# Performance work log

Measured on AMD Instinct MI355X. Metric: run time of the kernel, lower is better.

Reference implementation:

```python
import jax, jax.numpy as jnp
import numpy as np

N_U = 50000
N_I = 50000
E = 800000
HID = 64
HEADS = 4
OUT = 32
NEG_SLOPE = 0.2


def _gat(xs, xd, e, ws, wd, a_s, a_d, b, heads, ch, n_dst, concat):
    # xs:[Ns,Fin] xd:[Nd,Fin] e:[2,E]; PyG GATConv (no self loops, eval mode)
    hs = (xs @ ws).reshape(-1, heads, ch)  # [Ns,H,C]
    hd = (xd @ wd).reshape(-1, heads, ch)  # [Nd,H,C]
    al_s = jnp.einsum('nhc,hc->nh', hs, a_s)  # [Ns,H]
    al_d = jnp.einsum('nhc,hc->nh', hd, a_d)  # [Nd,H]
    src, dst = e[0], e[1]
    alpha = jax.nn.leaky_relu(al_s[src] + al_d[dst], NEG_SLOPE)  # [E,H]
    m = jax.lax.stop_gradient(jax.ops.segment_max(alpha, dst, num_segments=n_dst))
    ealpha = jnp.exp(alpha - m[dst])
    denom = jax.ops.segment_sum(ealpha, dst, num_segments=n_dst)
    coef = ealpha / (denom[dst] + 1e-16)  # segment softmax over incoming edges
    msg = hs[src] * coef[:, :, None]  # [E,H,C]
    out = jax.ops.segment_sum(msg, dst, num_segments=n_dst)  # [Nd,H,C]
    out = out.reshape(n_dst, heads * ch) if concat else out.mean(axis=1)
    return out + b


def _forward(x_user, x_item, e_u2i, e_i2u,
             p_user_w, p_user_b, p_item_w, p_item_b,
             l0_u2i_ws, l0_u2i_wd, l0_u2i_as, l0_u2i_ad, l0_u2i_b,
             l0_i2u_ws, l0_i2u_wd, l0_i2u_as, l0_i2u_ad, l0_i2u_b,
             l1_u2i_ws, l1_u2i_wd, l1_u2i_as, l1_u2i_ad, l1_u2i_b,
             l1_i2u_ws, l1_i2u_wd, l1_i2u_as, l1_i2u_ad, l1_i2u_b):
    hu = jax.nn.elu(x_user @ p_user_w + p_user_b)
    hi = jax.nn.elu(x_item @ p_item_w + p_item_b)
    # layer 0: heads=4, concat=True, out dim HID*HEADS; HeteroConv sum (one edge type per dst)
    hi1 = _gat(hu, hi, e_u2i, l0_u2i_ws, l0_u2i_wd, l0_u2i_as, l0_u2i_ad, l0_u2i_b, HEADS, HID, N_I, True)
    hu1 = _gat(hi, hu, e_i2u, l0_i2u_ws, l0_i2u_wd, l0_i2u_as, l0_i2u_ad, l0_i2u_b, HEADS, HID, N_U, True)
    hu1 = jax.nn.elu(hu1)  # dropout is identity in eval mode
    hi1 = jax.nn.elu(hi1)
    # layer 1: heads=1, concat=False -> mean over heads
    hi2 = _gat(hu1, hi1, e_u2i, l1_u2i_ws, l1_u2i_wd, l1_u2i_as, l1_u2i_ad, l1_u2i_b, 1, OUT, N_I, False)
    hu2 = _gat(hi1, hu1, e_i2u, l1_i2u_ws, l1_i2u_wd, l1_i2u_as, l1_i2u_ad, l1_i2u_b, 1, OUT, N_U, False)
    return hu2, hi2


def setup_inputs() -> dict:
    key = jax.random.key(0)
    ks = jax.random.split(key, 32)
    s = 0.1
    d = {
        'x_user': jax.random.normal(ks[0], (N_U, 128), jnp.float32),
        'x_item': jax.random.normal(ks[1], (N_I, 128), jnp.float32),
        'e_u2i': jax.random.randint(ks[2], (2, E), 0, 50000, jnp.int32),
        'e_i2u': jax.random.randint(ks[3], (2, E), 0, 50000, jnp.int32),
        'p_user_w': jax.random.normal(ks[4], (128, HID), jnp.float32) * s,
        'p_user_b': jax.random.normal(ks[5], (HID,), jnp.float32) * s,
        'p_item_w': jax.random.normal(ks[6], (128, HID), jnp.float32) * s,
        'p_item_b': jax.random.normal(ks[7], (HID,), jnp.float32) * s,
    }
    i = 8
    for lname, fin, h, c in (('l0', HID, HEADS, HID), ('l1', HID * HEADS, 1, OUT)):
        for et in ('u2i', 'i2u'):
            odim = h * c if lname == 'l0' else c
            d[f'{lname}_{et}_ws'] = jax.random.normal(ks[i], (fin, h * c), jnp.float32) * s; i += 1
            d[f'{lname}_{et}_wd'] = jax.random.normal(ks[i], (fin, h * c), jnp.float32) * s; i += 1
            d[f'{lname}_{et}_as'] = jax.random.normal(ks[i], (h, c), jnp.float32) * s; i += 1
            d[f'{lname}_{et}_ad'] = jax.random.normal(ks[i], (h, c), jnp.float32) * s; i += 1
            d[f'{lname}_{et}_b'] = jax.random.normal(ks[i], (odim,), jnp.float32) * s; i += 1
    return d


def reference(x_user, x_item, e_u2i, e_i2u,
              p_user_w, p_user_b, p_item_w, p_item_b,
              l0_u2i_ws, l0_u2i_wd, l0_u2i_as, l0_u2i_ad, l0_u2i_b,
              l0_i2u_ws, l0_i2u_wd, l0_i2u_as, l0_i2u_ad, l0_i2u_b,
              l1_u2i_ws, l1_u2i_wd, l1_u2i_as, l1_u2i_ad, l1_u2i_b,
              l1_i2u_ws, l1_i2u_wd, l1_i2u_as, l1_i2u_ad, l1_i2u_b):
    return _forward(x_user, x_item, e_u2i, e_i2u,
                    p_user_w, p_user_b, p_item_w, p_item_b,
                    l0_u2i_ws, l0_u2i_wd, l0_u2i_as, l0_u2i_ad, l0_u2i_b,
                    l0_i2u_ws, l0_i2u_wd, l0_i2u_as, l0_i2u_ad, l0_i2u_b,
                    l1_u2i_ws, l1_u2i_wd, l1_u2i_as, l1_u2i_ad, l1_u2i_b,
                    l1_i2u_ws, l1_i2u_wd, l1_i2u_as, l1_i2u_ad, l1_i2u_b)
```

## Files before the change

### kernel.cpp

```cpp
#include <hip/hip_runtime.h>
#include <cstdint>
#include <cstddef>

#define NN 50000
#define NE 800000
#define GB 196
#define TILE1 4096
#define CAP 8192

typedef __attribute__((ext_vector_type(8))) short short8;
typedef __attribute__((ext_vector_type(4))) float floatx4;

__device__ __forceinline__ float lrelu_f(float x){ return x >= 0.f ? x : 0.2f*x; }
__device__ __forceinline__ float elu_f(float x){ return x > 0.f ? x : __expf(x) - 1.f; }

__device__ __forceinline__ unsigned short f2bf(float f){
  unsigned int u = __float_as_uint(f);
  u += 0x7FFFu + ((u >> 16) & 1u);
  return (unsigned short)(u >> 16);
}
__device__ __forceinline__ float bf2f(unsigned int us){
  return __uint_as_float(us << 16);
}
__device__ __forceinline__ float4 bf4_load(const unsigned short* p){
  uint2 q = *(const uint2*)p;
  return make_float4(bf2f(q.x & 0xffffu), bf2f(q.x >> 16),
                     bf2f(q.y & 0xffffu), bf2f(q.y >> 16));
}
__device__ __forceinline__ uint2 bf4_pack(float4 o){
  uint2 p;
  p.x = (unsigned)f2bf(o.x) | ((unsigned)f2bf(o.y) << 16);
  p.y = (unsigned)f2bf(o.z) | ((unsigned)f2bf(o.w) << 16);
  return p;
}
__device__ __forceinline__ void split_bf(float a, unsigned short& h, unsigned short& l){
  h = f2bf(a);
  l = f2bf(a - bf2f(h));
}

__device__ __forceinline__ float dot2bf(float acc, unsigned a, unsigned b){
  asm("v_dot2_f32_bf16 %0, %1, %2, %0" : "+v"(acc) : "v"(a), "v"(b));
  return acc;
}

__global__ __launch_bounds__(256) void ghist_kernel(const int* __restrict__ e0,
                                                    const int* __restrict__ e1,
                                                    int* __restrict__ ghist){
  const int ty = blockIdx.y;
  const int* e = ty ? e1 : e0;
  __shared__ int h[GB];
  for (int j=threadIdx.x; j<GB; j+=256) h[j]=0;
  __syncthreads();
  for (int i = blockIdx.x*256 + threadIdx.x; i < NE; i += 256*256)
    atomicAdd(&h[e[NE+i]>>8], 1);
  __syncthreads();
  for (int j=threadIdx.x; j<GB; j+=256) if (h[j]) atomicAdd(&ghist[ty*200+j], h[j]);
}

__global__ __launch_bounds__(256) void gscan_kernel(const int* __restrict__ ghist,
                                                    int* __restrict__ gbase,
                                                    int* __restrict__ gcur){
  __shared__ int wb[4];
  const int t = threadIdx.x, wv = t>>6, l = t&63;
  for (int ty=0; ty<2; ++ty){
    int v = (t < GB) ? ghist[ty*200+t] : 0;
    int sum = v;
    #pragma unroll
    for (int off=1; off<64; off<<=1){
      int x = __shfl_up(sum, off, 64);
      if (l >= off) sum += x;
    }
    if (l == 63) wb[wv] = sum;
    __syncthreads();
    int wbase = 0;
    #pragma unroll
    for (int w=0; w<4; ++w) if (w < wv) wbase += wb[w];
    int excl = wbase + sum - v;
    if (t <= GB) gbase[ty*200+t] = excl;
    if (t <  GB) gcur [ty*200+t] = excl;
    __syncthreads();
  }
}

__global__ __launch_bounds__(256) void part1_kernel(const int* __restrict__ e0,
                                                    const int* __restrict__ e1,
                                                    int* __restrict__ gcur,
                                                    int2* __restrict__ p0,
                                                    int2* __restrict__ p1){
  const int ty = blockIdx.y;
  const int* e = ty ? e1 : e0;
  int2* pairs = ty ? p1 : p0;
  __shared__ int cnt[256];
  __shared__ int lstart[256];
  __shared__ int lcur[256];
  __shared__ int curg[GB];
  __shared__ int lsrc[TILE1];
  __shared__ int ldst[TILE1];
  __shared__ int wb[4];
  const int t = threadIdx.x;
  cnt[t] = 0;
  __syncthreads();
  int dreg[16], sreg[16];
  const int base = blockIdx.x*TILE1;
  const int ntile = min(TILE1, NE - base);
  #pragma unroll
  for (int it=0; it<16; ++it){
    int i = base + it*256 + t;
    int d = -1, s = 0;
    if (i < NE){ d = e[NE+i]; s = e[i]; atomicAdd(&cnt[d>>8], 1); }
    dreg[it] = d; sreg[it] = s;
  }
  __syncthreads();
  int c = cnt[t], sum = c;
  #pragma unroll
  for (int off=1; off<64; off<<=1){
    int x = __shfl_up(sum, off, 64);
    if ((t&63) >= off) sum += x;
  }
  if ((t&63) == 63) wb[t>>6] = sum;
  __syncthreads();
  int wbase = 0;
  #pragma unroll
  for (int w=0; w<4; ++w) if (w < (t>>6)) wbase += wb[w];
  int excl = wbase + sum - c;
  lstart[t] = excl;
  lcur[t] = excl;
  if (t < GB && c > 0) curg[t] = atomicAdd(&gcur[ty*200+t], c);
  __syncthreads();
  #pragma unroll
  for (int it=0; it<16; ++it){
    int d = dreg[it];
    if (d >= 0){
      int pos = atomicAdd(&lcur[d>>8], 1);
      lsrc[pos] = sreg[it];
      ldst[pos] = d;
    }
  }
  __syncthreads();
  for (int i=t; i<ntile; i+=256){
    int d = ldst[i];
    int j = d>>8;
    pairs[curg[j] + (i - lstart[j])] = make_int2(lsrc[i], d);
  }
}

struct Part2Job {
  const int2* pairs; const int* gbase;
  const float* als; const float* ald;
  int* ssrc; int* offs; unsigned short* coef;
};
__global__ __launch_bounds__(256) void part2_kernel(Part2Job j0, Part2Job j1){
  const Part2Job jb = blockIdx.y ? j1 : j0;
  const int b = blockIdx.x;
  const int t = threadIdx.x;
  __shared__ int lcnt[256];
  __shared__ int lcur[256];
  __shared__ int wb[4];
  __shared__ int sorted_src[CAP];
  __shared__ unsigned char sorted_dl[CAP];
  const int gb0 = jb.gbase[b], gb1 = jb.gbase[b+1];
  const int n = gb1 - gb0;
  lcnt[t] = 0;
  __syncthreads();
  for (int i=t; i<n; i+=256)
    atomicAdd(&lcnt[jb.pairs[gb0+i].y - (b<<8)], 1);
  __syncthreads();
  int c = lcnt[t], sum = c;
  #pragma unroll
  for (int off=1; off<64; off<<=1){
    int x = __shfl_up(sum, off, 64);
    if ((t&63) >= off) sum += x;
  }
  if ((t&63) == 63) wb[t>>6] = sum;
  __syncthreads();
  int wbase = 0;
  #pragma unroll
  for (int w=0; w<4; ++w) if (w < (t>>6)) wbase += wb[w];
  int excl = wbase + sum - c;
  lcur[t] = excl;
  int g = (b<<8) + t;
  if (g <= NN) jb.offs[g] = gb0 + excl;
  __syncthreads();
  for (int i=t; i<n; i+=256){
    int2 pr = jb.pairs[gb0+i];
    int dl = pr.y - (b<<8);
    int pos = atomicAdd(&lcur[dl], 1);
    sorted_src[pos] = pr.x;
    sorted_dl[pos] = (unsigned char)dl;
  }
  __syncthreads();
  const float4* als4 = (const float4*)jb.als;
  const float4* ald4 = (const float4*)jb.ald;
  for (int i=t; i<n; i+=256){
    int s  = sorted_src[i];
    int dl = sorted_dl[i];
    float4 a  = als4[s];
    float4 ad = ald4[(b<<8)+dl];
    float4 w;
    w.x = __expf(lrelu_f(a.x+ad.x));
    w.y = __expf(lrelu_f(a.y+ad.y));
    w.z = __expf(lrelu_f(a.z+ad.z));
    w.w = __expf(lrelu_f(a.w+ad.w));
    ((uint2*)jb.coef)[gb0+i] = bf4_pack(w);
    jb.ssrc[gb0+i] = s;
  }
}

struct MgJob {
  const void* A; const float* W; const float* bias;
  void* C; float* outA; float* outB;
  const float* cwS; const float* cwD;
};
template<int NT, bool ELU, bool BF16OUT, bool BF16A, bool LG, bool LOGIT>
__global__ __launch_bounds__(256) void mgemm_kernel(MgJob j0, MgJob j1,
                                                    int M, int K, int N)
{
  const MgJob jb = blockIdx.z ? j1 : j0;
  constexpr int TN = NT*16;
  __shared__ __align__(16) unsigned short Ah[64*72];
  __shared__ __align__(16) unsigned short Al[BF16A ? 8 : 64*72];
  __shared__ __align__(16) unsigned short Bh[TN*72];
  __shared__ __align__(16) unsigned short Bl[TN*72];
  __shared__ float CwS[LOGIT ? 256 : 1];
  __shared__ float CwD[LOGIT ? 256 : 1];
  const int t = threadIdx.x;
  const int m0 = blockIdx.x*64;
  const int n0 = blockIdx.y*TN;
  const int wv = t>>6, l = t&63;
  const int lr = l&15, lq = l>>4;
  if constexpr (LOGIT){ CwS[t] = jb.cwS[t]; CwD[t] = jb.cwD[t]; }
  floatx4 acc[NT];
  #pragma unroll
  for (int i=0;i<NT;i++) acc[i] = (floatx4){0.f,0.f,0.f,0.f};

  for (int kt=0; kt<K; kt+=64){
    if constexpr (BF16A){
      const unsigned short* A = (const unsigned short*)jb.A;
      #pragma unroll
      for (int i=0;i<2;i++){
        int li = t + i*256;
        int r = li >> 3, c8 = (li & 7)*8;
        short8 v = {0,0,0,0,0,0,0,0};
        if (m0 + r < M) v = *(const short8*)(A + (size_t)(m0+r)*K + kt + c8);
        *(short8*)&Ah[r*72 + c8] = v;
      }
    } else {
      const float* A = (const float*)jb.A;
      #pragma unroll
      for (int i=0;i<4;i++){
        int li = t + i*256;
        int r = li >> 4, c4 = (li & 15)*4;
        float4 v = make_float4(0.f,0.f,0.f,0.f);
        if (m0 + r < M) v = *(const float4*)(A + (size_t)(m0+r)*K + kt + c4);
        unsigned short h0,h1,h2,h3,g0,g1,g2,g3;
        split_bf(v.x,h0,g0); split_bf(v.y,h1,g1);
        split_bf(v.z,h2,g2); split_bf(v.w,h3,g3);
        uint2 ph = { (unsigned)h0 | ((unsigned)h1<<16), (unsigned)h2 | ((unsigned)h3<<16) };
        uint2 pl = { (unsigned)g0 | ((unsigned)g1<<16), (unsigned)g2 | ((unsigned)g3<<16) };
        *(uint2*)&Ah[r*72 + c4] = ph;
        *(uint2*)&Al[r*72 + c4] = pl;
      }
    }
    #pragma unroll
    for (int i=0;i<NT;i++){
      int li = t + i*256;
      int k  = li / (TN/4);
      int n4 = (li % (TN/4))*4;
      float4 v = *(const float4*)(jb.W + (size_t)(kt+k)*N + n0 + n4);
      unsigned short h, g;
      split_bf(v.x,h,g); Bh[(n4+0)*72+k]=h; Bl[(n4+0)*72+k]=g;
      split_bf(v.y,h,g); Bh[(n4+1)*72+k]=h; Bl[(n4+1)*72+k]=g;
      split_bf(v.z,h,g); Bh[(n4+2)*72+k]=h; Bl[(n4+2)*72+k]=g;
      split_bf(v.w,h,g); Bh[(n4+3)*72+k]=h; Bl[(n4+3)*72+k]=g;
    }
    __syncthreads();
    #pragma unroll
    for (int ks=0; ks<2; ks++){
      const int koff = ks*32 + lq*8;
      short8 a_h = *(const short8*)&Ah[(wv*16+lr)*72 + koff];
      short8 a_l;
      if constexpr (!BF16A) a_l = *(const short8*)&Al[(wv*16+lr)*72 + koff];
      #pragma unroll
      for (int nt=0; nt<NT; nt++){
        short8 b_h = *(const short8*)&Bh[(nt*16+lr)*72 + koff];
        short8 b_l = *(const short8*)&Bl[(nt*16+lr)*72 + koff];
        acc[nt] = __builtin_amdgcn_mfma_f32_16x16x32_bf16(a_h, b_h, acc[nt], 0,0,0);
        acc[nt] = __builtin_amdgcn_mfma_f32_16x16x32_bf16(a_h, b_l, acc[nt], 0,0,0);
        if constexpr (!BF16A)
          acc[nt] = __builtin_amdgcn_mfma_f32_16x16x32_bf16(a_l, b_h, acc[nt], 0,0,0);
      }
    }
    __syncthreads();
  }
  float ls[LOGIT ? 4 : 1][LOGIT ? 4 : 1];
  float ld_[LOGIT ? 4 : 1][LOGIT ? 4 : 1];
  if constexpr (LOGIT){
    #pragma unroll
    for (int r=0;r<4;r++)
      #pragma unroll
      for (int h=0;h<4;h++){ ls[r][h]=0.f; ld_[r][h]=0.f; }
  }
  #pragma unroll
  for (int nt=0; nt<NT; nt++){
    int n = n0 + nt*16 + lr;
    float bv = jb.bias ? jb.bias[n] : 0.f;
    #pragma unroll
    for (int r=0;r<4;r++){
      int m = m0 + wv*16 + lq*4 + r;
      if (m < M){
        float o = acc[nt][r] + bv;
        if (ELU) o = elu_f(o);
        if constexpr (LG){
          if (n < 32)       ((unsigned short*)jb.C)[(size_t)m*32 + n] = f2bf(o);
          else if (n == 32) jb.outA[m] = o;
          else if (n == 33) jb.outB[m] = o;
        } else {
          if (BF16OUT) ((unsigned short*)jb.C)[(size_t)m*N + n] = f2bf(o);
          else         ((float*)jb.C)[(size_t)m*N + n] = o;
        }
        if constexpr (LOGIT){
          #pragma unroll
          for (int h=0;h<4;h++){
            ls[r][h]  = fmaf(o, CwS[h*64 + n], ls[r][h]);
            ld_[r][h] = fmaf(o, CwD[h*64 + n], ld_[r][h]);
          }
        }
      }
    }
  }
  if constexpr (LOGIT){
    #pragma unroll
    for (int r=0;r<4;r++)
      #pragma unroll
      for (int h=0;h<4;h++){
        float a = ls[r][h], d = ld_[r][h];
        #pragma unroll
        for (int off=1; off<16; off<<=1){
          a += __shfl_xor(a, off, 64);
          d += __shfl_xor(d, off, 64);
        }
        ls[r][h]=a; ld_[r][h]=d;
      }
    if (lr == 0){
      #pragma unroll
      for (int r=0;r<4;r++){
        int m = m0 + wv*16 + lq*4 + r;
        if (m < M){
          #pragma unroll
          for (int h=0;h<4;h++){
            jb.outA[(size_t)m*4 + h] = ls[r][h];
            jb.outB[(size_t)m*4 + h] = ld_[r][h];
          }
        }
      }
    }
  }
}

struct HgJob {
  const unsigned short* A; const float* W; const float* den;
  const float* bias; unsigned short* out;
};
__global__ __launch_bounds__(256) void hgemm_kernel(HgJob j0, HgJob j1){
  const HgJob jb = blockIdx.z ? j1 : j0;
  const int head = blockIdx.y;
  const int m0 = blockIdx.x*64;
  __shared__ __align__(16) unsigned short Ah[64*72];
  __shared__ __align__(16) unsigned short Bh[64*72];
  __shared__ __align__(16) unsigned short Bl[64*72];
  const int t = threadIdx.x;
  const int wv = t>>6, l = t&63;
  const int lr = l&15, lq = l>>4;
  floatx4 acc[4];
  #pragma unroll
  for (int i=0;i<4;i++) acc[i] = (floatx4){0.f,0.f,0.f,0.f};
  #pragma unroll
  for (int i=0;i<2;i++){
    int li = t + i*256;
    int r = li >> 3, c8 = (li & 7)*8;
    short8 v = {0,0,0,0,0,0,0,0};
    if (m0 + r < NN) v = *(const short8*)(jb.A + (size_t)(m0+r)*256 + head*64 + c8);
    *(short8*)&Ah[r*72 + c8] = v;
  }
  #pragma unroll
  for (int i=0;i<4;i++){
    int li = t + i*256;
    int k  = li >> 4;
    int n4 = (li & 15)*4;
    float4 v = *(const float4*)(jb.W + (size_t)k*256 + head*64 + n4);
    unsigned short h, g;
    split_bf(v.x,h,g); Bh[(n4+0)*72+k]=h; Bl[(n4+0)*72+k]=g;
    split_bf(v.y,h,g); Bh[(n4+1)*72+k]=h; Bl[(n4+1)*72+k]=g;
    split_bf(v.z,h,g); Bh[(n4+2)*72+k]=h; Bl[(n4+2)*72+k]=g;
    split_bf(v.w,h,g); Bh[(n4+3)*72+k]=h; Bl[(n4+3)*72+k]=g;
  }
  __syncthreads();
  #pragma unroll
  for (int ks=0; ks<2; ks++){
    const int koff = ks*32 + lq*8;
    short8 a_h = *(const short8*)&Ah[(wv*16+lr)*72 + koff];
    #pragma unroll
    for (int nt=0; nt<4; nt++){
      short8 b_h = *(const short8*)&Bh[(nt*16+lr)*72 + koff];
      short8 b_l = *(const short8*)&Bl[(nt*16+lr)*72 + koff];
      acc[nt] = __builtin_amdgcn_mfma_f32_16x16x32_bf16(a_h, b_h, acc[nt], 0,0,0);
      acc[nt] = __builtin_amdgcn_mfma_f32_16x16x32_bf16(a_h, b_l, acc[nt], 0,0,0);
    }
  }
  float inv[4];
  #pragma unroll
  for (int r=0;r<4;r++){
    int m = m0 + wv*16 + lq*4 + r;
    inv[r] = (m < NN) ? 1.f/(jb.den[(size_t)m*4 + head] + 1e-16f) : 0.f;
  }
  #pragma unroll
  for (int nt=0; nt<4; nt++){
    int col = head*64 + nt*16 + lr;
    float bv = jb.bias[col];
    #pragma unroll
    for (int r=0;r<4;r++){
      int m = m0 + wv*16 + lq*4 + r;
      if (m < NN)
        jb.out[(size_t)m*256 + col] = f2bf(elu_f(acc[nt][r]*inv[r] + bv));
    }
  }
}

struct CollapseJob { const float* W; const float* a; float* out; int K,H,C; };
struct CollapseArgs { CollapseJob j[8]; };
__global__ void collapse_kernel(CollapseArgs args){
  CollapseJob jb = args.j[blockIdx.x];
  int t = threadIdx.x;
  if (t < jb.K * jb.H){
    int k = t / jb.H, h = t % jb.H;
    const float* wr = jb.W + (size_t)k * (jb.H*jb.C) + h*jb.C;
    const float* ar = jb.a + h*jb.C;
    float s = 0.f;
    for (int c=0;c<jb.C;c++) s += wr[c]*ar[c];
    jb.out[h*jb.K + k] = s;
  }
}

__global__ __launch_bounds__(256) void prep1_kernel(
    const float* __restrict__ WsA, const float* __restrict__ cwSA, const float* __restrict__ cwDA,
    const float* __restrict__ WsB, const float* __restrict__ cwSB, const float* __restrict__ cwDB,
    float* __restrict__ WcA, float* __restrict__ WcB){
  const float* Ws  = blockIdx.x ? WsB  : WsA;
  const float* cwS = blockIdx.x ? cwSB : cwSA;
  const float* cwD = blockIdx.x ? cwDB : cwDA;
  float* Wc = blockIdx.x ? WcB : WcA;
  const int k = threadIdx.x;
  #pragma unroll
  for (int n=0;n<32;n++) Wc[(size_t)k*48 + n] = Ws[(size_t)k*32 + n];
  Wc[(size_t)k*48 + 32] = cwS[k];
  Wc[(size_t)k*48 + 33] = cwD[k];
  #pragma unroll
  for (int n=34;n<48;n++) Wc[(size_t)k*48 + n] = 0.f;
}

struct AggPJob {
  const int* offs; const int* ssrc;
  const unsigned short* x;
  const unsigned short* coef;
  unsigned short* agg;
  float* den;
};
__global__ __launch_bounds__(256) void aggpre_kernel(AggPJob ja, AggPJob jbb){
  const AggPJob jb = blockIdx.y ? jbb : ja;
  const int tid = threadIdx.x;
  const int lane = tid & 63, wid = tid >> 6;
  const int grp = lane >> 3;
  const int cl  = lane & 7;
  const int c8  = cl * 8;
  const int dst = blockIdx.x*32 + wid*8 + grp;
  if (dst >= NN) return;
  const int b0 = jb.offs[dst], b1 = jb.offs[dst+1];
  float acc[4][8];
  float den[4] = {0.f,0.f,0.f,0.f};
  #pragma unroll
  for (int h=0;h<4;h++)
    #pragma unroll
    for (int c=0;c<8;c++) acc[h][c]=0.f;
  const unsigned ONE2 = 0x3F803F80u;
  int e = b0;
  for (; e+1 < b1; e += 2){
    int s0 = jb.ssrc[e];
    int s1 = jb.ssrc[e+1];
    uint4 q0 = *(const uint4*)(jb.x + ((size_t)s0<<6) + c8);
    uint4 q1 = *(const uint4*)(jb.x + ((size_t)s1<<6) + c8);
    uint2 w0 = *(const uint2*)(jb.coef + (size_t)e*4);
    uint2 w1 = *(const uint2*)(jb.coef + (size_t)(e+1)*4);
    unsigned wp[4];
    wp[0] = __builtin_amdgcn_perm(w1.x, w0.x, 0x05040100u);
    wp[1] = __builtin_amdgcn_perm(w1.x, w0.x, 0x07060302u);
    wp[2] = __builtin_amdgcn_perm(w1.y, w0.y, 0x05040100u);
    wp[3] = __builtin_amdgcn_perm(w1.y, w0.y, 0x07060302u);
    unsigned xp[8];
    xp[0] = __builtin_amdgcn_perm(q1.x, q0.x, 0x05040100u);
    xp[1] = __builtin_amdgcn_perm(q1.x, q0.x, 0x07060302u);
    xp[2] = __builtin_amdgcn_perm(q1.y, q0.y, 0x05040100u);
    xp[3] = __builtin_amdgcn_perm(q1.y, q0.y, 0x07060302u);
    xp[4] = __builtin_amdgcn_perm(q1.z, q0.z, 0x05040100u);
    xp[5] = __builtin_amdgcn_perm(q1.z, q0.z, 0x07060302u);
    xp[6] = __builtin_amdgcn_perm(q1.w, q0.w, 0x05040100u);
    xp[7] = __builtin_amdgcn_perm(q1.w, q0.w, 0x07060302u);
    #pragma unroll
    for (int h=0;h<4;h++){
      den[h] = dot2bf(den[h], wp[h], ONE2);
      #pragma unroll
      for (int c=0;c<8;c++) acc[h][c] = dot2bf(acc[h][c], wp[h], xp[c]);
    }
  }
  if (e < b1){
    int s = jb.ssrc[e];
    uint4 q = *(const uint4*)(jb.x + ((size_t)s<<6) + c8);
    uint2 w = *(const uint2*)(jb.coef + (size_t)e*4);
    float wf[4] = { bf2f(w.x & 0xffffu), bf2f(w.x >> 16),
                    bf2f(w.y & 0xffffu), bf2f(w.y >> 16) };
    float xf[8] = { bf2f(q.x & 0xffffu), bf2f(q.x >> 16),
                    bf2f(q.y & 0xffffu), bf2f(q.y >> 16),
                    bf2f(q.z & 0xffffu), bf2f(q.z >> 16),
                    bf2f(q.w & 0xffffu), bf2f(q.w >> 16) };
    #pragma unroll
    for (int h=0;h<4;h++){
      den[h] += wf[h];
      #pragma unroll
      for (int c=0;c<8;c++) acc[h][c] += wf[h]*xf[c];
    }
  }
  #pragma unroll
  for (int h=0;h<4;h++){
    uint2 plo = bf4_pack(make_float4(acc[h][0],acc[h][1],acc[h][2],acc[h][3]));
    uint2 phi = bf4_pack(make_float4(acc[h][4],acc[h][5],acc[h][6],acc[h][7]));
    uint4 pk = { plo.x, plo.y, phi.x, phi.y };
    *(uint4*)(jb.agg + (size_t)dst*256 + h*64 + c8) = pk;
  }
  if (cl == 0)
    *(float4*)(jb.den + (size_t)dst*4) = make_float4(den[0],den[1],den[2],den[3]);
}

struct Agg1Job {
  const int* offs; const int* ssrc;
  const unsigned short* hs;
  const float* als; const float* ald;
  const float* bias; float* out;
};
__global__ __launch_bounds__(256) void agg1_kernel(Agg1Job ja, Agg1Job jbb){
  const Agg1Job jb = blockIdx.y ? jbb : ja;
  const int wid = threadIdx.x>>6, lane = threadIdx.x&63;
  const int dst = blockIdx.x*4 + wid;
  if (dst >= NN) return;
  const int b0 = jb.offs[dst], b1 = jb.offs[dst+1];
  const float ad = jb.ald[dst];
  const int slot = lane>>3, c4 = (lane&7)*4;
  float4 acc = make_float4(0.f,0.f,0.f,0.f);
  float den = 0.f;
  int e = b0 + slot;
  for (; e+8 < b1; e += 16){
    int s0 = jb.ssrc[e], s1 = jb.ssrc[e+8];
    float a0 = jb.als[s0];
    float a1 = jb.als[s1];
    float4 v0 = bf4_load(jb.hs + ((size_t)s0<<5) + c4);
    float4 v1 = bf4_load(jb.hs + ((size_t)s1<<5) + c4);
    float w0 = __expf(lrelu_f(a0 + ad));
    float w1 = __expf(lrelu_f(a1 + ad));
    acc.x += w0*v0.x + w1*v1.x;
    acc.y += w0*v0.y + w1*v1.y;
    acc.z += w0*v0.z + w1*v1.z;
    acc.w += w0*v0.w + w1*v1.w;
    den += w0 + w1;
  }
  if (e < b1){
    int s = jb.ssrc[e];
    float w = __expf(lrelu_f(jb.als[s] + ad));
    float4 v = bf4_load(jb.hs + ((size_t)s<<5) + c4);
    acc.x += w*v.x; acc.y += w*v.y; acc.z += w*v.z; acc.w += w*v.w;
    den += w;
  }
  #pragma unroll
  for (int off=32; off>=8; off>>=1){
    acc.x += __shfl_xor(acc.x, off, 64);
    acc.y += __shfl_xor(acc.y, off, 64);
    acc.z += __shfl_xor(acc.z, off, 64);
    acc.w += __shfl_xor(acc.w, off, 64);
    den   += __shfl_xor(den,   off, 64);
  }
  if (lane < 8){
    const float inv = 1.f/(den + 1e-16f);
    float4 b = *(const float4*)(jb.bias + c4);
    float4 o = make_float4(acc.x*inv+b.x, acc.y*inv+b.y, acc.z*inv+b.z, acc.w*inv+b.w);
    *(float4*)(jb.out + (size_t)dst*32 + c4) = o;
  }
}

extern "C" void kernel_launch(void* const* d_in, const int* in_sizes, int n_in,
                              void* d_out, int out_size, void* d_ws, size_t ws_size,
                              hipStream_t stream)
{
  (void)in_sizes; (void)n_in; (void)out_size; (void)ws_size;
  const float* x_user   = (const float*)d_in[0];
  const float* x_item   = (const float*)d_in[1];
  const int*   e_u2i    = (const int*)  d_in[2];
  const int*   e_i2u    = (const int*)  d_in[3];
  const float* p_user_w = (const float*)d_in[4];
  const float* p_user_b = (const float*)d_in[5];
  const float* p_item_w = (const float*)d_in[6];
  const float* p_item_b = (const float*)d_in[7];
  const float* l0_u2i_ws=(const float*)d_in[8];
  const float* l0_u2i_wd=(const float*)d_in[9];
  const float* l0_u2i_as=(const float*)d_in[10];
  const float* l0_u2i_ad=(const float*)d_in[11];
  const float* l0_u2i_b =(const float*)d_in[12];
  const float* l0_i2u_ws=(const float*)d_in[13];
  const float* l0_i2u_wd=(const float*)d_in[14];
  const float* l0_i2u_as=(const float*)d_in[15];
  const float* l0_i2u_ad=(const float*)d_in[16];
  const float* l0_i2u_b =(const float*)d_in[17];
  const float* l1_u2i_ws=(const float*)d_in[18];
  const float* l1_u2i_wd=(const float*)d_in[19];
  const float* l1_u2i_as=(const float*)d_in[20];
  const float* l1_u2i_ad=(const float*)d_in[21];
  const float* l1_u2i_b =(const float*)d_in[22];
  const float* l1_i2u_ws=(const float*)d_in[23];
  const float* l1_i2u_wd=(const float*)d_in[24];
  const float* l1_i2u_as=(const float*)d_in[25];
  const float* l1_i2u_ad=(const float*)d_in[26];
  const float* l1_i2u_b =(const float*)d_in[27];

  char* base = (char*)d_ws;
  size_t off = 0;
  auto alloc = [&](size_t bytes)->void*{
    void* p = base + off;
    off += (bytes + 255) & ~(size_t)255;
    return p;
  };
  int* offs_u2i = (int*)alloc((size_t)(NN+1)*sizeof(int));
  int* offs_i2u = (int*)alloc((size_t)(NN+1)*sizeof(int));
  int* ssrc_u2i = (int*)alloc((size_t)NE*sizeof(int));
  int* ssrc_i2u = (int*)alloc((size_t)NE*sizeof(int));
  int* ghist    = (int*)alloc((size_t)2*200*sizeof(int));
  int* gbase    = (int*)alloc((size_t)2*200*sizeof(int));
  int* gcur     = (int*)alloc((size_t)2*200*sizeof(int));
  unsigned short* coef0_u2i = (unsigned short*)alloc((size_t)NE*4*sizeof(unsigned short));
  unsigned short* coef0_i2u = (unsigned short*)alloc((size_t)NE*4*sizeof(unsigned short));
  unsigned short* hu = (unsigned short*)alloc((size_t)NN*64*sizeof(unsigned short));
  unsigned short* hi = (unsigned short*)alloc((size_t)NN*64*sizeof(unsigned short));
  unsigned short* agg_u2i = (unsigned short*)alloc((size_t)NN*256*sizeof(unsigned short));
  unsigned short* agg_i2u = (unsigned short*)alloc((size_t)NN*256*sizeof(unsigned short));
  float* den_u2i = (float*)alloc((size_t)NN*4*sizeof(float));
  float* den_i2u = (float*)alloc((size_t)NN*4*sizeof(float));
  unsigned short* hu1 = (unsigned short*)alloc((size_t)NN*256*sizeof(unsigned short));
  unsigned short* hi1 = (unsigned short*)alloc((size_t)NN*256*sizeof(unsigned short));
  unsigned short* hs1_u2i = (unsigned short*)alloc((size_t)NN*32*sizeof(unsigned short));
  unsigned short* hs1_i2u = (unsigned short*)alloc((size_t)NN*32*sizeof(unsigned short));
  float* als0_u2i = (float*)alloc((size_t)NN*4*sizeof(float));
  float* ald0_u2i = (float*)alloc((size_t)NN*4*sizeof(float));
  float* als0_i2u = (float*)alloc((size_t)NN*4*sizeof(float));
  float* ald0_i2u = (float*)alloc((size_t)NN*4*sizeof(float));
  float* als1_u2i = (float*)alloc((size_t)NN*sizeof(float));
  float* ald1_u2i = (float*)alloc((size_t)NN*sizeof(float));
  float* als1_i2u = (float*)alloc((size_t)NN*sizeof(float));
  float* ald1_i2u = (float*)alloc((size_t)NN*sizeof(float));
  float* cw0s_u2i = (float*)alloc(256*sizeof(float));
  float* cw0d_u2i = (float*)alloc(256*sizeof(float));
  float* cw0s_i2u = (float*)alloc(256*sizeof(float));
  float* cw0d_i2u = (float*)alloc(256*sizeof(float));
  float* cw1s_u2i = (float*)alloc(256*sizeof(float));
  float* cw1d_u2i = (float*)alloc(256*sizeof(float));
  float* cw1s_i2u = (float*)alloc(256*sizeof(float));
  float* cw1d_i2u = (float*)alloc(256*sizeof(float));
  float* Wc_u2i   = (float*)alloc((size_t)256*48*sizeof(float));
  float* Wc_i2u   = (float*)alloc((size_t)256*48*sizeof(float));
  int2* pairs_u2i = (int2*)hu1;
  int2* pairs_i2u = pairs_u2i + NE;

  const int GM = (NN + 63)/64;

  hipMemsetAsync(ghist, 0, (size_t)2*200*sizeof(int), stream);
  ghist_kernel<<<dim3(256,2), 256, 0, stream>>>(e_u2i, e_i2u, ghist);
  gscan_kernel<<<1, 256, 0, stream>>>(ghist, gbase, gcur);
  part1_kernel<<<dim3((NE+TILE1-1)/TILE1,2), 256, 0, stream>>>(
      e_u2i, e_i2u, gcur, pairs_u2i, pairs_i2u);

  CollapseArgs ca;
  ca.j[0] = {l0_u2i_ws, l0_u2i_as, cw0s_u2i, 64, 4, 64};
  ca.j[1] = {l0_u2i_wd, l0_u2i_ad, cw0d_u2i, 64, 4, 64};
  ca.j[2] = {l0_i2u_ws, l0_i2u_as, cw0s_i2u, 64, 4, 64};
  ca.j[3] = {l0_i2u_wd, l0_i2u_ad, cw0d_i2u, 64, 4, 64};
  ca.j[4] = {l1_u2i_ws, l1_u2i_as, cw1s_u2i, 256, 1, 32};
  ca.j[5] = {l1_u2i_wd, l1_u2i_ad, cw1d_u2i, 256, 1, 32};
  ca.j[6] = {l1_i2u_ws, l1_i2u_as, cw1s_i2u, 256, 1, 32};
  ca.j[7] = {l1_i2u_wd, l1_i2u_ad, cw1d_i2u, 256, 1, 32};
  collapse_kernel<<<8, 256, 0, stream>>>(ca);

  mgemm_kernel<4,true,true,false,false,true><<<dim3(GM,1,2), 256, 0, stream>>>(
      MgJob{x_user, p_user_w, p_user_b, hu, als0_u2i, ald0_i2u, cw0s_u2i, cw0d_i2u},
      MgJob{x_item, p_item_w, p_item_b, hi, als0_i2u, ald0_u2i, cw0s_i2u, cw0d_u2i},
      NN, 128, 64);

  prep1_kernel<<<2, 256, 0, stream>>>(
      l1_u2i_ws, cw1s_u2i, cw1d_i2u,
      l1_i2u_ws, cw1s_i2u, cw1d_u2i,
      Wc_u2i, Wc_i2u);

  part2_kernel<<<dim3(GB,2), 256, 0, stream>>>(
      Part2Job{pairs_u2i, gbase,       als0_u2i, ald0_u2i, ssrc_u2i, offs_u2i, coef0_u2i},
      Part2Job{pairs_i2u, gbase + 200, als0_i2u, ald0_i2u, ssrc_i2u, offs_i2u, coef0_i2u});

  aggpre_kernel<<<dim3((NN+31)/32,2), 256, 0, stream>>>(
      AggPJob{offs_u2i, ssrc_u2i, hu, coef0_u2i, agg_u2i, den_u2i},
      AggPJob{offs_i2u, ssrc_i2u, hi, coef0_i2u, agg_i2u, den_i2u});

  hgemm_kernel<<<dim3(GM,4,2), 256, 0, stream>>>(
      HgJob{agg_u2i, l0_u2i_ws, den_u2i, l0_u2i_b, hi1},
      HgJob{agg_i2u, l0_i2u_ws, den_i2u, l0_i2u_b, hu1});

  mgemm_kernel<3,false,true,true,true,false><<<dim3(GM,1,2), 256, 0, stream>>>(
      MgJob{hu1, Wc_u2i, nullptr, hs1_u2i, als1_u2i, ald1_i2u, nullptr, nullptr},
      MgJob{hi1, Wc_i2u, nullptr, hs1_i2u, als1_i2u, ald1_u2i, nullptr, nullptr},
      NN, 256, 48);

  float* hu2 = (float*)d_out;
  float* hi2 = (float*)d_out + (size_t)NN*32;
  agg1_kernel<<<dim3(NN/4,2), 256, 0, stream>>>(
      Agg1Job{offs_u2i, ssrc_u2i, hs1_u2i, als1_u2i, ald1_u2i, l1_u2i_b, hi2},
      Agg1Job{offs_i2u, ssrc_i2u, hs1_i2u, als1_i2u, ald1_i2u, l1_i2u_b, hu2});
}
```

Measured before the change: 398.5 us.

## Pre-split weights to transposed bf16 hi/lo once and load MFMA operands directly

Adds a single weight-conversion kernel that splits every GEMM weight into transposed bf16 high and low parts once, replacing the per-block fp32 split and LDS transpose in both GEMM kernels. The GEMM kernels drop shared-memory staging and the barriers that go with it, loading A and B MFMA fragments straight from global memory in register layout. The aim is to remove redundant per-block conversion work and LDS traffic. In exchange each wave issues uncoalesced strided global loads and reuses data through cache instead of LDS, and one extra small kernel launch is added.

New measurement: 448.1 us. +12.4%, slower.

```diff
diff --git a/kernel.cpp b/kernel.cpp
--- a/kernel.cpp
+++ b/kernel.cpp
@@ -206,21 +206,45 @@
   }
 }
 
+struct WcvJob {
+  const float* W; const float* cwS; const float* cwD;
+  unsigned short* Wth; unsigned short* Wtl;
+  int K; int N; int mode;
+};
+struct WcvArgs { WcvJob j[6]; };
+__global__ __launch_bounds__(256) void wconv_kernel(WcvArgs args){
+  WcvJob jb = args.j[blockIdx.y];
+  int idx = blockIdx.x*256 + threadIdx.x;
+  if (idx >= jb.K * jb.N) return;
+  int k = idx / jb.N, n = idx % jb.N;
+  float val;
+  if (jb.mode == 0) val = jb.W[(size_t)k*jb.N + n];
+  else {
+    if (n < 32)       val = jb.W[(size_t)k*32 + n];
+    else if (n == 32) val = jb.cwS[k];
+    else if (n == 33) val = jb.cwD[k];
+    else              val = 0.f;
+  }
+  unsigned short h, g;
+  split_bf(val, h, g);
+  jb.Wth[(size_t)n*jb.K + k] = h;
+  jb.Wtl[(size_t)n*jb.K + k] = g;
+}
+
 struct MgJob {
-  const void* A; const float* W; const float* bias;
+  const void* A;
+  const unsigned short* Wth;
+  const unsigned short* Wtl;
+  const float* bias;
   void* C; float* outA; float* outB;
   const float* cwS; const float* cwD;
 };
-template<int NT, bool ELU, bool BF16OUT, bool BF16A, bool LG, bool LOGIT>
+template<int NT, int KK, bool ELU, bool BF16OUT, bool F32A, bool LG, bool LOGIT>
 __global__ __launch_bounds__(256) void mgemm_kernel(MgJob j0, MgJob j1,
-                                                    int M, int K, int N)
+                                                    int M, int N)
 {
   const MgJob jb = blockIdx.z ? j1 : j0;
   constexpr int TN = NT*16;
-  __shared__ __align__(16) unsigned short Ah[64*72];
-  __shared__ __align__(16) unsigned short Al[BF16A ? 8 : 64*72];
-  __shared__ __align__(16) unsigned short Bh[TN*72];
-  __shared__ __align__(16) unsigned short Bl[TN*72];
   __shared__ float CwS[LOGIT ? 256 : 1];
   __shared__ float CwD[LOGIT ? 256 : 1];
   const int t = threadIdx.x;
@@ -233,65 +257,44 @@
   #pragma unroll
   for (int i=0;i<NT;i++) acc[i] = (floatx4){0.f,0.f,0.f,0.f};
 
-  for (int kt=0; kt<K; kt+=64){
-    if constexpr (BF16A){
-      const unsigned short* A = (const unsigned short*)jb.A;
-      #pragma unroll
-      for (int i=0;i<2;i++){
-        int li = t + i*256;
-        int r = li >> 3, c8 = (li & 7)*8;
-        short8 v = {0,0,0,0,0,0,0,0};
-        if (m0 + r < M) v = *(const short8*)(A + (size_t)(m0+r)*K + kt + c8);
-        *(short8*)&Ah[r*72 + c8] = v;
+  int arow = m0 + wv*16 + lr;
+  if (arow >= M) arow = M-1;
+
+  #pragma unroll
+  for (int kt=0; kt<KK; kt+=64){
+    #pragma unroll
+    for (int ks=0; ks<2; ks++){
+      const int koff = kt + ks*32 + lq*8;
+      short8 a_h, a_l;
+      if constexpr (F32A){
+        const float* Af = (const float*)jb.A;
+        float4 u0 = *(const float4*)(Af + (size_t)arow*KK + koff);
+        float4 u1 = *(const float4*)(Af + (size_t)arow*KK + koff + 4);
+        float vv[8] = {u0.x,u0.y,u0.z,u0.w,u1.x,u1.y,u1.z,u1.w};
+        union { unsigned short u[8]; short8 v; } AH, AL;
+        #pragma unroll
+        for (int j=0;j<8;j++){
+          unsigned short hh, gg;
+          split_bf(vv[j], hh, gg);
+          AH.u[j] = hh; AL.u[j] = gg;
+        }
+        a_h = AH.v; a_l = AL.v;
+      } else {
+        a_h = *(const short8*)((const unsigned short*)jb.A + (size_t)arow*KK + koff);
       }
-    } else {
-      const float* A = (const float*)jb.A;
-      #pragma unroll
-      for (int i=0;i<4;i++){
-        int li = t + i*256;
-        int r = li >> 4, c4 = (li & 15)*4;
-        float4 v = make_float4(0.f,0.f,0.f,0.f);
-        if (m0 + r < M) v = *(const float4*)(A + (size_t)(m0+r)*K + kt + c4);
-        unsigned short h0,h1,h2,h3,g0,g1,g2,g3;
-        split_bf(v.x,h0,g0); split_bf(v.y,h1,g1);
-        split_bf(v.z,h2,g2); split_bf(v.w,h3,g3);
-        uint2 ph = { (unsigned)h0 | ((unsigned)h1<<16), (unsigned)h2 | ((unsigned)h3<<16) };
-        uint2 pl = { (unsigned)g0 | ((unsigned)g1<<16), (unsigned)g2 | ((unsigned)g3<<16) };
-        *(uint2*)&Ah[r*72 + c4] = ph;
-        *(uint2*)&Al[r*72 + c4] = pl;
-      }
-    }
-    #pragma unroll
-    for (int i=0;i<NT;i++){
-      int li = t + i*256;
-      int k  = li / (TN/4);
-      int n4 = (li % (TN/4))*4;
-      float4 v = *(const float4*)(jb.W + (size_t)(kt+k)*N + n0 + n4);
-      unsigned short h, g;
-      split_bf(v.x,h,g); Bh[(n4+0)*72+k]=h; Bl[(n4+0)*72+k]=g;
-      split_bf(v.y,h,g); Bh[(n4+1)*72+k]=h; Bl[(n4+1)*72+k]=g;
-      split_bf(v.z,h,g); Bh[(n4+2)*72+k]=h; Bl[(n4+2)*72+k]=g;
-      split_bf(v.w,h,g); Bh[(n4+3)*72+k]=h; Bl[(n4+3)*72+k]=g;
-    }
-    __syncthreads();
-    #pragma unroll
-    for (int ks=0; ks<2; ks++){
-      const int koff = ks*32 + lq*8;
-      short8 a_h = *(const short8*)&Ah[(wv*16+lr)*72 + koff];
-      short8 a_l;
-      if constexpr (!BF16A) a_l = *(const short8*)&Al[(wv*16+lr)*72 + koff];
       #pragma unroll
       for (int nt=0; nt<NT; nt++){
-        short8 b_h = *(const short8*)&Bh[(nt*16+lr)*72 + koff];
-        short8 b_l = *(const short8*)&Bl[(nt*16+lr)*72 + koff];
+        const size_t boff = (size_t)(n0 + nt*16 + lr)*KK + koff;
+        short8 b_h = *(const short8*)(jb.Wth + boff);
+        short8 b_l = *(const short8*)(jb.Wtl + boff);
         acc[nt] = __builtin_amdgcn_mfma_f32_16x16x32_bf16(a_h, b_h, acc[nt], 0,0,0);
         acc[nt] = __builtin_amdgcn_mfma_f32_16x16x32_bf16(a_h, b_l, acc[nt], 0,0,0);
-        if constexpr (!BF16A)
+        if constexpr (F32A)
           acc[nt] = __builtin_amdgcn_mfma_f32_16x16x32_bf16(a_l, b_h, acc[nt], 0,0,0);
       }
     }
-    __syncthreads();
-  }
+  }
+  if constexpr (LOGIT) __syncthreads();
   float ls[LOGIT ? 4 : 1][LOGIT ? 4 : 1];
   float ld_[LOGIT ? 4 : 1][LOGIT ? 4 : 1];
   if constexpr (LOGIT){
@@ -358,51 +361,33 @@
 }
 
 struct HgJob {
-  const unsigned short* A; const float* W; const float* den;
+  const unsigned short* A;
+  const unsigned short* Wth;
+  const unsigned short* Wtl;
+  const float* den;
   const float* bias; unsigned short* out;
 };
 __global__ __launch_bounds__(256) void hgemm_kernel(HgJob j0, HgJob j1){
   const HgJob jb = blockIdx.z ? j1 : j0;
   const int head = blockIdx.y;
   const int m0 = blockIdx.x*64;
-  __shared__ __align__(16) unsigned short Ah[64*72];
-  __shared__ __align__(16) unsigned short Bh[64*72];
-  __shared__ __align__(16) unsigned short Bl[64*72];
   const int t = threadIdx.x;
   const int wv = t>>6, l = t&63;
   const int lr = l&15, lq = l>>4;
   floatx4 acc[4];
   #pragma unroll
   for (int i=0;i<4;i++) acc[i] = (floatx4){0.f,0.f,0.f,0.f};
-  #pragma unroll
-  for (int i=0;i<2;i++){
-    int li = t + i*256;
-    int r = li >> 3, c8 = (li & 7)*8;
-    short8 v = {0,0,0,0,0,0,0,0};
-    if (m0 + r < NN) v = *(const short8*)(jb.A + (size_t)(m0+r)*256 + head*64 + c8);
-    *(short8*)&Ah[r*72 + c8] = v;
-  }
-  #pragma unroll
-  for (int i=0;i<4;i++){
-    int li = t + i*256;
-    int k  = li >> 4;
-    int n4 = (li & 15)*4;
-    float4 v = *(const float4*)(jb.W + (size_t)k*256 + head*64 + n4);
-    unsigned short h, g;
-    split_bf(v.x,h,g); Bh[(n4+0)*72+k]=h; Bl[(n4+0)*72+k]=g;
-    split_bf(v.y,h,g); Bh[(n4+1)*72+k]=h; Bl[(n4+1)*72+k]=g;
-    split_bf(v.z,h,g); Bh[(n4+2)*72+k]=h; Bl[(n4+2)*72+k]=g;
-    split_bf(v.w,h,g); Bh[(n4+3)*72+k]=h; Bl[(n4+3)*72+k]=g;
-  }
-  __syncthreads();
+  int arow = m0 + wv*16 + lr;
+  if (arow >= NN) arow = NN-1;
   #pragma unroll
   for (int ks=0; ks<2; ks++){
     const int koff = ks*32 + lq*8;
-    short8 a_h = *(const short8*)&Ah[(wv*16+lr)*72 + koff];
+    short8 a_h = *(const short8*)(jb.A + (size_t)arow*256 + head*64 + koff);
     #pragma unroll
     for (int nt=0; nt<4; nt++){
-      short8 b_h = *(const short8*)&Bh[(nt*16+lr)*72 + koff];
-      short8 b_l = *(const short8*)&Bl[(nt*16+lr)*72 + koff];
+      const size_t boff = (size_t)(head*64 + nt*16 + lr)*64 + koff;
+      short8 b_h = *(const short8*)(jb.Wth + boff);
+      short8 b_l = *(const short8*)(jb.Wtl + boff);
       acc[nt] = __builtin_amdgcn_mfma_f32_16x16x32_bf16(a_h, b_h, acc[nt], 0,0,0);
       acc[nt] = __builtin_amdgcn_mfma_f32_16x16x32_bf16(a_h, b_l, acc[nt], 0,0,0);
     }
@@ -439,23 +424,6 @@
     for (int c=0;c<jb.C;c++) s += wr[c]*ar[c];
     jb.out[h*jb.K + k] = s;
   }
-}
-
-__global__ __launch_bounds__(256) void prep1_kernel(
-    const float* __restrict__ WsA, const float* __restrict__ cwSA, const float* __restrict__ cwDA,
-    const float* __restrict__ WsB, const float* __restrict__ cwSB, const float* __restrict__ cwDB,
-    float* __restrict__ WcA, float* __restrict__ WcB){
-  const float* Ws  = blockIdx.x ? WsB  : WsA;
-  const float* cwS = blockIdx.x ? cwSB : cwSA;
-  const float* cwD = blockIdx.x ? cwDB : cwDA;
-  float* Wc = blockIdx.x ? WcB : WcA;
-  const int k = threadIdx.x;
-  #pragma unroll
-  for (int n=0;n<32;n++) Wc[(size_t)k*48 + n] = Ws[(size_t)k*32 + n];
-  Wc[(size_t)k*48 + 32] = cwS[k];
-  Wc[(size_t)k*48 + 33] = cwD[k];
-  #pragma unroll
-  for (int n=34;n<48;n++) Wc[(size_t)k*48 + n] = 0.f;
 }
 
 struct AggPJob {
@@ -669,8 +637,18 @@
   float* cw1d_u2i = (float*)alloc(256*sizeof(float));
   float* cw1s_i2u = (float*)alloc(256*sizeof(float));
   float* cw1d_i2u = (float*)alloc(256*sizeof(float));
-  float* Wc_u2i   = (float*)alloc((size_t)256*48*sizeof(float));
-  float* Wc_i2u   = (float*)alloc((size_t)256*48*sizeof(float));
+  unsigned short* wt_pu_h  = (unsigned short*)alloc((size_t)64*128*sizeof(unsigned short));
+  unsigned short* wt_pu_l  = (unsigned short*)alloc((size_t)64*128*sizeof(unsigned short));
+  unsigned short* wt_pi_h  = (unsigned short*)alloc((size_t)64*128*sizeof(unsigned short));
+  unsigned short* wt_pi_l  = (unsigned short*)alloc((size_t)64*128*sizeof(unsigned short));
+  unsigned short* wt_l0u_h = (unsigned short*)alloc((size_t)256*64*sizeof(unsigned short));
+  unsigned short* wt_l0u_l = (unsigned short*)alloc((size_t)256*64*sizeof(unsigned short));
+  unsigned short* wt_l0i_h = (unsigned short*)alloc((size_t)256*64*sizeof(unsigned short));
+  unsigned short* wt_l0i_l = (unsigned short*)alloc((size_t)256*64*sizeof(unsigned short));
+  unsigned short* wt_wcu_h = (unsigned short*)alloc((size_t)48*256*sizeof(unsigned short));
+  unsigned short* wt_wcu_l = (unsigned short*)alloc((size_t)48*256*sizeof(unsigned short));
+  unsigned short* wt_wci_h = (unsigned short*)alloc((size_t)48*256*sizeof(unsigned short));
+  unsigned short* wt_wci_l = (unsigned short*)alloc((size_t)48*256*sizeof(unsigned short));
   int2* pairs_u2i = (int2*)hu1;
   int2* pairs_i2u = pairs_u2i + NE;
 
@@ -693,15 +671,19 @@
   ca.j[7] = {l1_i2u_wd, l1_i2u_ad, cw1d_i2u, 256, 1, 32};
   collapse_kernel<<<8, 256, 0, stream>>>(ca);
 
-  mgemm_kernel<4,true,true,false,false,true><<<dim3(GM,1,2), 256, 0, stream>>>(
-      MgJob{x_user, p_user_w, p_user_b, hu, als0_u2i, ald0_i2u, cw0s_u2i, cw0d_i2u},
-      MgJob{x_item, p_item_w, p_item_b, hi, als0_i2u, ald0_u2i, cw0s_i2u, cw0d_u2i},
-      NN, 128, 64);
-
-  prep1_kernel<<<2, 256, 0, stream>>>(
-      l1_u2i_ws, cw1s_u2i, cw1d_i2u,
-      l1_i2u_ws, cw1s_i2u, cw1d_u2i,
-      Wc_u2i, Wc_i2u);
+  WcvArgs wa;
+  wa.j[0] = {p_user_w,  nullptr,   nullptr,   wt_pu_h,  wt_pu_l,  128, 64, 0};
+  wa.j[1] = {p_item_w,  nullptr,   nullptr,   wt_pi_h,  wt_pi_l,  128, 64, 0};
+  wa.j[2] = {l0_u2i_ws, nullptr,   nullptr,   wt_l0u_h, wt_l0u_l, 64, 256, 0};
+  wa.j[3] = {l0_i2u_ws, nullptr,   nullptr,   wt_l0i_h, wt_l0i_l, 64, 256, 0};
+  wa.j[4] = {l1_u2i_ws, cw1s_u2i,  cw1d_i2u,  wt_wcu_h, wt_wcu_l, 256, 48, 1};
+  wa.j[5] = {l1_i2u_ws, cw1s_i2u,  cw1d_u2i,  wt_wci_h, wt_wci_l, 256, 48, 1};
+  wconv_kernel<<<dim3(64,6), 256, 0, stream>>>(wa);
+
+  mgemm_kernel<4,128,true,true,true,false,true><<<dim3(GM,1,2), 256, 0, stream>>>(
+      MgJob{x_user, wt_pu_h, wt_pu_l, p_user_b, hu, als0_u2i, ald0_i2u, cw0s_u2i, cw0d_i2u},
+      MgJob{x_item, wt_pi_h, wt_pi_l, p_item_b, hi, als0_i2u, ald0_u2i, cw0s_i2u, cw0d_u2i},
+      NN, 64);
 
   part2_kernel<<<dim3(GB,2), 256, 0, stream>>>(
       Part2Job{pairs_u2i, gbase,       als0_u2i, ald0_u2i, ssrc_u2i, offs_u2i, coef0_u2i},
@@ -712,13 +694,13 @@
       AggPJob{offs_i2u, ssrc_i2u, hi, coef0_i2u, agg_i2u, den_i2u});
 
   hgemm_kernel<<<dim3(GM,4,2), 256, 0, stream>>>(
-      HgJob{agg_u2i, l0_u2i_ws, den_u2i, l0_u2i_b, hi1},
-      HgJob{agg_i2u, l0_i2u_ws, den_i2u, l0_i2u_b, hu1});
-
-  mgemm_kernel<3,false,true,true,true,false><<<dim3(GM,1,2), 256, 0, stream>>>(
-      MgJob{hu1, Wc_u2i, nullptr, hs1_u2i, als1_u2i, ald1_i2u, nullptr, nullptr},
-      MgJob{hi1, Wc_i2u, nullptr, hs1_i2u, als1_i2u, ald1_u2i, nullptr, nullptr},
-      NN, 256, 48);
+      HgJob{agg_u2i, wt_l0u_h, wt_l0u_l, den_u2i, l0_u2i_b, hi1},
+      HgJob{agg_i2u, wt_l0i_h, wt_l0i_l, den_i2u, l0_i2u_b, hu1});
+
+  mgemm_kernel<3,256,false,true,false,true,false><<<dim3(GM,1,2), 256, 0, stream>>>(
+      MgJob{hu1, wt_wcu_h, wt_wcu_l, nullptr, hs1_u2i, als1_u2i, ald1_i2u, nullptr, nullptr},
+      MgJob{hi1, wt_wci_h, wt_wci_l, nullptr, hs1_i2u, als1_i2u, ald1_u2i, nullptr, nullptr},
+      NN, 48);
 
   float* hu2 = (float*)d_out;
   float* hi2 = (float*)d_out + (size_t)NN*32;
```
